# Performance work log

Hardware: AMD Instinct MI355X
Metric: run time of the kernel (lower is better)

The kernel has to match this reference:

```python
import jax, jax.numpy as jnp
import numpy as np

TAU = 1.0
MAX_ITER = 10


def setup_inputs() -> dict:
    key = jax.random.key(0)
    s = jax.random.normal(key, (32, 1024, 1024), dtype=jnp.float32)
    return {"s": s}


def reference(s) -> jnp.ndarray:
    # s: [B, N1, N2] with N1 <= N2 (square here), no padding -> fully vectorized
    log_s = s / TAU
    for i in range(MAX_ITER):
        # even iter: row normalization (logsumexp over columns, axis=2)
        # odd  iter: column normalization (logsumexp over rows, axis=1)
        axis = 2 if i % 2 == 0 else 1
        log_s = log_s - jax.nn.logsumexp(log_s, axis=axis, keepdims=True)
    return jnp.exp(log_s)
```

## Files before the change

kernel.cpp:

```cpp
#include <hip/hip_runtime.h>
#include <math.h>


#define BATCH 32
#define N 1024
#define CHUNKS 8
#define ROWS_PER_CHUNK (N / CHUNKS)

__global__ __launch_bounds__(256) void zero_c_kernel(float* __restrict__ c) {
    int idx = blockIdx.x * 256 + threadIdx.x;
    c[idx] = 0.0f;
}

__global__ __launch_bounds__(256) void row_lse_kernel(const float* __restrict__ s,
                                                      const float* __restrict__ c,
                                                      float* __restrict__ r) {
    const int wave = threadIdx.x >> 6;
    const int lane = threadIdx.x & 63;
    const int row  = blockIdx.x * 4 + wave;
    const int b    = row >> 10;

    const float4* __restrict__ srow = (const float4*)(s + (size_t)row * N);
    const float4* __restrict__ crow = (const float4*)(c + (size_t)b * N);

    float x[16];
#pragma unroll
    for (int k = 0; k < 4; k++) {
        float4 v  = srow[lane + k * 64];
        float4 cv = crow[lane + k * 64];
        x[4 * k + 0] = v.x + cv.x;
        x[4 * k + 1] = v.y + cv.y;
        x[4 * k + 2] = v.z + cv.z;
        x[4 * k + 3] = v.w + cv.w;
    }

    float m = x[0];
#pragma unroll
    for (int t = 1; t < 16; t++) m = fmaxf(m, x[t]);
#pragma unroll
    for (int off = 32; off > 0; off >>= 1) m = fmaxf(m, __shfl_xor(m, off, 64));

    float sum = 0.0f;
#pragma unroll
    for (int t = 0; t < 16; t++) sum += __expf(x[t] - m);
#pragma unroll
    for (int off = 32; off > 0; off >>= 1) sum += __shfl_xor(sum, off, 64);

    if (lane == 0) r[row] = -(m + __logf(sum));
}

__global__ __launch_bounds__(1024) void col_lse_partial_kernel(const float* __restrict__ s,
                                                               const float* __restrict__ r,
                                                               float* __restrict__ pm,
                                                               float* __restrict__ pl) {
    const int bc    = blockIdx.x;
    const int b     = bc >> 3;
    const int chunk = bc & (CHUNKS - 1);
    const int j     = threadIdx.x;

    __shared__ float rs[ROWS_PER_CHUNK];
    if (threadIdx.x < ROWS_PER_CHUNK)
        rs[threadIdx.x] = r[b * N + chunk * ROWS_PER_CHUNK + threadIdx.x];
    __syncthreads();

    const float* __restrict__ base =
        s + ((size_t)(b * N + chunk * ROWS_PER_CHUNK)) * N + j;

    float m = -3.0e38f, l = 0.0f;
#pragma unroll 4
    for (int i = 0; i < ROWS_PER_CHUNK; i++) {
        float x  = base[(size_t)i * N] + rs[i];
        float mn = fmaxf(m, x);
        l = l * __expf(m - mn) + __expf(x - mn);
        m = mn;
    }
    pm[bc * N + j] = m;
    pl[bc * N + j] = l;
}

__global__ __launch_bounds__(1024) void col_combine_kernel(const float* __restrict__ pm,
                                                           const float* __restrict__ pl,
                                                           float* __restrict__ c) {
    const int b = blockIdx.x;
    const int j = threadIdx.x;
    float M = -3.0e38f, L = 0.0f;
#pragma unroll
    for (int chunk = 0; chunk < CHUNKS; chunk++) {
        float m  = pm[(b * CHUNKS + chunk) * N + j];
        float l  = pl[(b * CHUNKS + chunk) * N + j];
        float mn = fmaxf(M, m);
        L = L * __expf(M - mn) + l * __expf(m - mn);
        M = mn;
    }
    c[b * N + j] = -(M + __logf(L));
}

__global__ __launch_bounds__(1024) void col_lse_direct_kernel(const float* __restrict__ s,
                                                              const float* __restrict__ r,
                                                              float* __restrict__ c) {
    const int b = blockIdx.x;
    const int j = threadIdx.x;
    const float* __restrict__ rb = r + b * N;
    const float* __restrict__ base = s + (size_t)b * N * N + j;
    float m = -3.0e38f, l = 0.0f;
    for (int i = 0; i < N; i++) {
        float x  = base[(size_t)i * N] + rb[i];
        float mn = fmaxf(m, x);
        l = l * __expf(m - mn) + __expf(x - mn);
        m = mn;
    }
    c[b * N + j] = -(m + __logf(l));
}

__global__ __launch_bounds__(256) void finalize_kernel(const float* __restrict__ s,
                                                       const float* __restrict__ r,
                                                       const float* __restrict__ c,
                                                       float* __restrict__ out) {
    const int f4  = blockIdx.x * 256 + threadIdx.x;
    const int j4  = f4 & 255;
    const int row = f4 >> 8;
    const int b   = row >> 10;

    float4 v  = ((const float4*)s)[f4];
    float  rr = r[row];
    float4 cc = ((const float4*)c)[(b << 8) + j4];

    float4 o;
    o.x = __expf(v.x + rr + cc.x);
    o.y = __expf(v.y + rr + cc.y);
    o.z = __expf(v.z + rr + cc.z);
    o.w = __expf(v.w + rr + cc.w);
    ((float4*)out)[f4] = o;
}

extern "C" void kernel_launch(void* const* d_in, const int* in_sizes, int n_in,
                              void* d_out, int out_size, void* d_ws, size_t ws_size,
                              hipStream_t stream) {
    const float* s = (const float*)d_in[0];
    float* out = (float*)d_out;

    float* c  = (float*)d_ws;
    float* r  = c + BATCH * N;
    float* pm = r + BATCH * N;
    float* pl = pm + BATCH * CHUNKS * N;

    const size_t needed = (size_t)(2 * BATCH * N + 2 * BATCH * CHUNKS * N) * sizeof(float);
    const bool use_partials = ws_size >= needed;

    zero_c_kernel<<<(BATCH * N) / 256, 256, 0, stream>>>(c);

    for (int it = 0; it < 10; it++) {
        if ((it & 1) == 0) {
            row_lse_kernel<<<(BATCH * N) / 4, 256, 0, stream>>>(s, c, r);
        } else if (use_partials) {
            col_lse_partial_kernel<<<BATCH * CHUNKS, 1024, 0, stream>>>(s, r, pm, pl);
            col_combine_kernel<<<BATCH, 1024, 0, stream>>>(pm, pl, c);
        } else {
            col_lse_direct_kernel<<<BATCH, 1024, 0, stream>>>(s, r, c);
        }
    }

    const int total_f4 = BATCH * N * N / 4;
    finalize_kernel<<<total_f4 / 256, 256, 0, stream>>>(s, r, c, out);
}
```

Baseline: 436.8 us.

## Fuse row LSE with column partial LSE per row-chunk block

Replaces separate row-normalization and column-partial kernels with one kernel per row chunk. It computes row LSEs for 32 rows, keeps them in shared memory, then rereads those rows (likely from cache) to build column partial max/sum with float4 loads. The combine kernel gains more parallelism via an intra-block tree, and the zero-init launch is removed. The workspace requirement grows to 32 partial chunks, and the fallback path becomes the slow direct column kernel.

```diff
diff --git a/kernel.cpp b/kernel.cpp
--- a/kernel.cpp
+++ b/kernel.cpp
@@ -4,12 +4,132 @@
 
 #define BATCH 32
 #define N 1024
-#define CHUNKS 8
-#define ROWS_PER_CHUNK (N / CHUNKS)
+#define RCHUNKS 32
+#define ROWS_PER_BLK 32
+#define BGROUPS 2
+#define ROWS_PER_GROUP 16
+#define PCHUNKS RCHUNKS
+
+__global__ __launch_bounds__(512, 4) void fused_pair_kernel(
+    const float* __restrict__ s, const float* __restrict__ c,
+    float* __restrict__ r, float* __restrict__ pm, float* __restrict__ pl,
+    int has_c)
+{
+    const int bc    = blockIdx.x;
+    const int b     = bc >> 5;
+    const int chunk = bc & 31;
+    const int row0  = chunk * ROWS_PER_BLK;
+
+    __shared__ float cs[N];
+    __shared__ float rs[ROWS_PER_BLK];
+    __shared__ float sm[BGROUPS][N];
+    __shared__ float sl[BGROUPS][N];
+
+    if (has_c) {
+        ((float2*)cs)[threadIdx.x] = ((const float2*)(c + b * N))[threadIdx.x];
+    } else {
+        ((float2*)cs)[threadIdx.x] = make_float2(0.f, 0.f);
+    }
+    __syncthreads();
+
+    const int wave = threadIdx.x >> 6;
+    const int lane = threadIdx.x & 63;
+    const float4* cs4 = (const float4*)cs;
+#pragma unroll
+    for (int rp = 0; rp < 4; rp++) {
+        const int row = wave * 4 + rp;
+        const float4* srow = (const float4*)(s + ((size_t)(b * N + row0 + row)) * N);
+        float x[16];
+#pragma unroll
+        for (int k = 0; k < 4; k++) {
+            float4 v  = srow[lane + 64 * k];
+            float4 cv = cs4[lane + 64 * k];
+            x[4*k+0] = v.x + cv.x; x[4*k+1] = v.y + cv.y;
+            x[4*k+2] = v.z + cv.z; x[4*k+3] = v.w + cv.w;
+        }
+        float m = x[0];
+#pragma unroll
+        for (int t = 1; t < 16; t++) m = fmaxf(m, x[t]);
+#pragma unroll
+        for (int off = 32; off > 0; off >>= 1) m = fmaxf(m, __shfl_xor(m, off, 64));
+        float sum = 0.f;
+#pragma unroll
+        for (int t = 0; t < 16; t++) sum += __expf(x[t] - m);
+#pragma unroll
+        for (int off = 32; off > 0; off >>= 1) sum += __shfl_xor(sum, off, 64);
+        if (lane == 0) {
+            float rv = -(m + __logf(sum));
+            rs[row] = rv;
+            r[b * N + row0 + row] = rv;
+        }
+    }
+    __syncthreads();
+
+    const int j4 = threadIdx.x & 255;
+    const int g  = threadIdx.x >> 8;
+    const float4* sb4 = (const float4*)(s + ((size_t)(b * N + row0 + g * ROWS_PER_GROUP)) * N);
+    float m0=-3.0e38f, m1=-3.0e38f, m2=-3.0e38f, m3=-3.0e38f;
+    float l0=0.f, l1=0.f, l2=0.f, l3=0.f;
+#pragma unroll
+    for (int i = 0; i < ROWS_PER_GROUP; i++) {
+        float ri = rs[g * ROWS_PER_GROUP + i];
+        float4 v = sb4[(size_t)i * 256 + j4];
+        float x0 = v.x + ri, x1 = v.y + ri, x2 = v.z + ri, x3 = v.w + ri;
+        float n0 = fmaxf(m0, x0); l0 = l0 * __expf(m0 - n0) + __expf(x0 - n0); m0 = n0;
+        float n1 = fmaxf(m1, x1); l1 = l1 * __expf(m1 - n1) + __expf(x1 - n1); m1 = n1;
+        float n2 = fmaxf(m2, x2); l2 = l2 * __expf(m2 - n2) + __expf(x2 - n2); m2 = n2;
+        float n3 = fmaxf(m3, x3); l3 = l3 * __expf(m3 - n3) + __expf(x3 - n3); m3 = n3;
+    }
+    ((float4*)sm[g])[j4] = make_float4(m0, m1, m2, m3);
+    ((float4*)sl[g])[j4] = make_float4(l0, l1, l2, l3);
+    __syncthreads();
+
+#pragma unroll
+    for (int cc = 0; cc < 2; cc++) {
+        const int col = threadIdx.x + cc * 512;
+        float M = sm[0][col], L = sl[0][col];
+        float m = sm[1][col], l = sl[1][col];
+        float mn = fmaxf(M, m);
+        L = L * __expf(M - mn) + l * __expf(m - mn);
+        pm[(size_t)bc * N + col] = mn;
+        pl[(size_t)bc * N + col] = L;
+    }
+}
+
+__global__ __launch_bounds__(1024) void col_combine_kernel(
+    const float* __restrict__ pm, const float* __restrict__ pl,
+    float* __restrict__ c)
+{
+    const int b  = blockIdx.x >> 2;
+    const int q  = blockIdx.x & 3;
+    const int jc = threadIdx.x & 255;
+    const int kg = threadIdx.x >> 8;
+    const int j  = q * 256 + jc;
+    float M = -3.0e38f, L = 0.f;
+#pragma unroll
+    for (int k = 0; k < 8; k++) {
+        const int kk = kg * 8 + k;
+        float m = pm[((size_t)(b * PCHUNKS + kk)) * N + j];
+        float l = pl[((size_t)(b * PCHUNKS + kk)) * N + j];
+        float mn = fmaxf(M, m);
+        L = L * __expf(M - mn) + l * __expf(m - mn); M = mn;
+    }
+    __shared__ float smm[4][256], sll[4][256];
+    smm[kg][jc] = M; sll[kg][jc] = L;
+    __syncthreads();
+    if (kg == 0) {
+#pragma unroll
+        for (int g2 = 1; g2 < 4; g2++) {
+            float m = smm[g2][jc], l = sll[g2][jc];
+            float mn = fmaxf(M, m);
+            L = L * __expf(M - mn) + l * __expf(m - mn); M = mn;
+        }
+        c[b * N + j] = -(M + __logf(L));
+    }
+}
 
 __global__ __launch_bounds__(256) void zero_c_kernel(float* __restrict__ c) {
-    int idx = blockIdx.x * 256 + threadIdx.x;
-    c[idx] = 0.0f;
+    c[blockIdx.x * 256 + threadIdx.x] = 0.0f;
 }
 
 __global__ __launch_bounds__(256) void row_lse_kernel(const float* __restrict__ s,
@@ -19,80 +139,26 @@
     const int lane = threadIdx.x & 63;
     const int row  = blockIdx.x * 4 + wave;
     const int b    = row >> 10;
-
-    const float4* __restrict__ srow = (const float4*)(s + (size_t)row * N);
-    const float4* __restrict__ crow = (const float4*)(c + (size_t)b * N);
-
+    const float4* srow = (const float4*)(s + (size_t)row * N);
+    const float4* crow = (const float4*)(c + (size_t)b * N);
     float x[16];
 #pragma unroll
     for (int k = 0; k < 4; k++) {
-        float4 v  = srow[lane + k * 64];
+        float4 v = srow[lane + k * 64];
         float4 cv = crow[lane + k * 64];
-        x[4 * k + 0] = v.x + cv.x;
-        x[4 * k + 1] = v.y + cv.y;
-        x[4 * k + 2] = v.z + cv.z;
-        x[4 * k + 3] = v.w + cv.w;
-    }
-
+        x[4*k+0]=v.x+cv.x; x[4*k+1]=v.y+cv.y; x[4*k+2]=v.z+cv.z; x[4*k+3]=v.w+cv.w;
+    }
     float m = x[0];
 #pragma unroll
     for (int t = 1; t < 16; t++) m = fmaxf(m, x[t]);
 #pragma unroll
     for (int off = 32; off > 0; off >>= 1) m = fmaxf(m, __shfl_xor(m, off, 64));
-
-    float sum = 0.0f;
+    float sum = 0.f;
 #pragma unroll
     for (int t = 0; t < 16; t++) sum += __expf(x[t] - m);
 #pragma unroll
     for (int off = 32; off > 0; off >>= 1) sum += __shfl_xor(sum, off, 64);
-
     if (lane == 0) r[row] = -(m + __logf(sum));
-}
-
-__global__ __launch_bounds__(1024) void col_lse_partial_kernel(const float* __restrict__ s,
-                                                               const float* __restrict__ r,
-                                                               float* __restrict__ pm,
-                                                               float* __restrict__ pl) {
-    const int bc    = blockIdx.x;
-    const int b     = bc >> 3;
-    const int chunk = bc & (CHUNKS - 1);
-    const int j     = threadIdx.x;
-
-    __shared__ float rs[ROWS_PER_CHUNK];
-    if (threadIdx.x < ROWS_PER_CHUNK)
-        rs[threadIdx.x] = r[b * N + chunk * ROWS_PER_CHUNK + threadIdx.x];
-    __syncthreads();
-
-    const float* __restrict__ base =
-        s + ((size_t)(b * N + chunk * ROWS_PER_CHUNK)) * N + j;
-
-    float m = -3.0e38f, l = 0.0f;
-#pragma unroll 4
-    for (int i = 0; i < ROWS_PER_CHUNK; i++) {
-        float x  = base[(size_t)i * N] + rs[i];
-        float mn = fmaxf(m, x);
-        l = l * __expf(m - mn) + __expf(x - mn);
-        m = mn;
-    }
-    pm[bc * N + j] = m;
-    pl[bc * N + j] = l;
-}
-
-__global__ __launch_bounds__(1024) void col_combine_kernel(const float* __restrict__ pm,
-                                                           const float* __restrict__ pl,
-                                                           float* __restrict__ c) {
-    const int b = blockIdx.x;
-    const int j = threadIdx.x;
-    float M = -3.0e38f, L = 0.0f;
-#pragma unroll
-    for (int chunk = 0; chunk < CHUNKS; chunk++) {
-        float m  = pm[(b * CHUNKS + chunk) * N + j];
-        float l  = pl[(b * CHUNKS + chunk) * N + j];
-        float mn = fmaxf(M, m);
-        L = L * __expf(M - mn) + l * __expf(m - mn);
-        M = mn;
-    }
-    c[b * N + j] = -(M + __logf(L));
 }
 
 __global__ __launch_bounds__(1024) void col_lse_direct_kernel(const float* __restrict__ s,
@@ -100,9 +166,9 @@
                                                               float* __restrict__ c) {
     const int b = blockIdx.x;
     const int j = threadIdx.x;
-    const float* __restrict__ rb = r + b * N;
-    const float* __restrict__ base = s + (size_t)b * N * N + j;
-    float m = -3.0e38f, l = 0.0f;
+    const float* rb = r + b * N;
+    const float* base = s + (size_t)b * N * N + j;
+    float m = -3.0e38f, l = 0.f;
     for (int i = 0; i < N; i++) {
         float x  = base[(size_t)i * N] + rb[i];
         float mn = fmaxf(m, x);
@@ -120,11 +186,9 @@
     const int j4  = f4 & 255;
     const int row = f4 >> 8;
     const int b   = row >> 10;
-
     float4 v  = ((const float4*)s)[f4];
     float  rr = r[row];
     float4 cc = ((const float4*)c)[(b << 8) + j4];
-
     float4 o;
     o.x = __expf(v.x + rr + cc.x);
     o.y = __expf(v.y + rr + cc.y);
@@ -142,21 +206,24 @@
     float* c  = (float*)d_ws;
     float* r  = c + BATCH * N;
     float* pm = r + BATCH * N;
-    float* pl = pm + BATCH * CHUNKS * N;
-
-    const size_t needed = (size_t)(2 * BATCH * N + 2 * BATCH * CHUNKS * N) * sizeof(float);
-    const bool use_partials = ws_size >= needed;
-
-    zero_c_kernel<<<(BATCH * N) / 256, 256, 0, stream>>>(c);
-
-    for (int it = 0; it < 10; it++) {
-        if ((it & 1) == 0) {
-            row_lse_kernel<<<(BATCH * N) / 4, 256, 0, stream>>>(s, c, r);
-        } else if (use_partials) {
-            col_lse_partial_kernel<<<BATCH * CHUNKS, 1024, 0, stream>>>(s, r, pm, pl);
-            col_combine_kernel<<<BATCH, 1024, 0, stream>>>(pm, pl, c);
-        } else {
-            col_lse_direct_kernel<<<BATCH, 1024, 0, stream>>>(s, r, c);
+    float* pl = pm + BATCH * PCHUNKS * N;
+
+    const size_t needed =
+        (size_t)(2 * BATCH * N + 2 * BATCH * PCHUNKS * N) * sizeof(float);
+
+    if (ws_size >= needed) {
+        for (int p = 0; p < 5; p++) {
+            fused_pair_kernel<<<BATCH * RCHUNKS, 512, 0, stream>>>(
+                s, c, r, pm, pl, p > 0 ? 1 : 0);
+            col_combine_kernel<<<BATCH * 4, 1024, 0, stream>>>(pm, pl, c);
+        }
+    } else {
+        zero_c_kernel<<<(BATCH * N) / 256, 256, 0, stream>>>(c);
+        for (int it = 0; it < 10; it++) {
+            if ((it & 1) == 0)
+                row_lse_kernel<<<(BATCH * N) / 4, 256, 0, stream>>>(s, c, r);
+            else
+                col_lse_direct_kernel<<<BATCH, 1024, 0, stream>>>(s, r, c);
         }
     }
 
```

Measured after the change: 431.7 us. Within noise of the previous version (-1.2%).

## Replace multi-kernel Sinkhorn loop with a persistent cooperative kernel using grid syncs

Applied to the files above, without the earlier changes.

Fuses all row and column log-sum-exp passes plus the final exp into one cooperative persistent kernel of 1024 blocks. Grid-wide syncs take the place of the roughly 17 separate kernel launches. Each block owns a 32-row by 32-column tile per batch, so the per-chunk data may stay resident in L2/MALL across iterations. Column reductions are combined within the block through shared memory instead of partial buffers and a combine kernel. This depends on all 1024 blocks being co-resident; if the cooperative launch fails, it falls back to the slower direct column kernel path.

```diff
diff --git a/kernel.cpp b/kernel.cpp
--- a/kernel.cpp
+++ b/kernel.cpp
@@ -1,15 +1,129 @@
 #include <hip/hip_runtime.h>
+#include <hip/hip_cooperative_groups.h>
 #include <math.h>
+
+namespace cg = cooperative_groups;
 
 
 #define BATCH 32
 #define N 1024
-#define CHUNKS 8
-#define ROWS_PER_CHUNK (N / CHUNKS)
+#define NBLOCKS 1024
+#define NTHREADS 256
+
+__global__ __launch_bounds__(256, 4) void sinkhorn_persistent(
+    const float* __restrict__ s, float* __restrict__ r, float* __restrict__ c,
+    float* __restrict__ out)
+{
+    cg::grid_group grid = cg::this_grid();
+    const int t     = threadIdx.x;
+    const int b     = blockIdx.x >> 5;
+    const int chunk = blockIdx.x & 31;
+
+    __shared__ float cs[N];
+    __shared__ float rs[N];
+    __shared__ float4 sm[32][8];
+    __shared__ float4 sl[32][8];
+
+    const int wave = t >> 6;
+    const int lane = t & 63;
+
+    for (int it = 0; it < 10; it += 2) {
+        if (it == 0)
+            ((float4*)cs)[t] = make_float4(0.f, 0.f, 0.f, 0.f);
+        else
+            ((float4*)cs)[t] = ((const float4*)(c + b * N))[t];
+        __syncthreads();
+        const float4* cs4 = (const float4*)cs;
+        for (int rp = 0; rp < 8; rp++) {
+            const int row = wave * 8 + rp;
+            const float4* srow =
+                (const float4*)(s + ((size_t)(b * N + chunk * 32 + row)) * N);
+            float x[16];
+#pragma unroll
+            for (int k = 0; k < 4; k++) {
+                float4 v  = srow[lane + 64 * k];
+                float4 cv = cs4[lane + 64 * k];
+                x[4*k+0] = v.x + cv.x; x[4*k+1] = v.y + cv.y;
+                x[4*k+2] = v.z + cv.z; x[4*k+3] = v.w + cv.w;
+            }
+            float m = x[0];
+#pragma unroll
+            for (int q = 1; q < 16; q++) m = fmaxf(m, x[q]);
+#pragma unroll
+            for (int off = 32; off; off >>= 1) m = fmaxf(m, __shfl_xor(m, off, 64));
+            float sum = 0.f;
+#pragma unroll
+            for (int q = 0; q < 16; q++) sum += __expf(x[q] - m);
+#pragma unroll
+            for (int off = 32; off; off >>= 1) sum += __shfl_xor(sum, off, 64);
+            if (lane == 0)
+                r[b * N + chunk * 32 + row] = -(m + __logf(sum));
+        }
+        grid.sync();
+
+        ((float4*)rs)[t] = ((const float4*)(r + b * N))[t];
+        __syncthreads();
+        const int col4 = t & 7;
+        const int rch  = t >> 3;
+        const float4* base =
+            (const float4*)(s + ((size_t)(b * N + rch * 32)) * N) + chunk * 8 + col4;
+        float4 m4 = make_float4(-3e38f, -3e38f, -3e38f, -3e38f);
+        float4 l4 = make_float4(0.f, 0.f, 0.f, 0.f);
+#pragma unroll 4
+        for (int i = 0; i < 32; i++) {
+            float ri = rs[rch * 32 + i];
+            float4 v = base[(size_t)i * 256];
+            float x0 = v.x + ri, x1 = v.y + ri, x2 = v.z + ri, x3 = v.w + ri;
+            float n;
+            n = fmaxf(m4.x, x0); l4.x = l4.x * __expf(m4.x - n) + __expf(x0 - n); m4.x = n;
+            n = fmaxf(m4.y, x1); l4.y = l4.y * __expf(m4.y - n) + __expf(x1 - n); m4.y = n;
+            n = fmaxf(m4.z, x2); l4.z = l4.z * __expf(m4.z - n) + __expf(x2 - n); m4.z = n;
+            n = fmaxf(m4.w, x3); l4.w = l4.w * __expf(m4.w - n) + __expf(x3 - n); m4.w = n;
+        }
+        sm[rch][col4] = m4;
+        sl[rch][col4] = l4;
+        __syncthreads();
+        if (t < 8) {
+            float4 M = sm[0][t], L = sl[0][t];
+#pragma unroll
+            for (int k2 = 1; k2 < 32; k2++) {
+                float4 m2 = sm[k2][t], l2 = sl[k2][t];
+                float n;
+                n = fmaxf(M.x, m2.x); L.x = L.x * __expf(M.x - n) + l2.x * __expf(m2.x - n); M.x = n;
+                n = fmaxf(M.y, m2.y); L.y = L.y * __expf(M.y - n) + l2.y * __expf(m2.y - n); M.y = n;
+                n = fmaxf(M.z, m2.z); L.z = L.z * __expf(M.z - n) + l2.z * __expf(m2.z - n); M.z = n;
+                n = fmaxf(M.w, m2.w); L.w = L.w * __expf(M.w - n) + l2.w * __expf(m2.w - n); M.w = n;
+            }
+            float4 o;
+            o.x = -(M.x + __logf(L.x));
+            o.y = -(M.y + __logf(L.y));
+            o.z = -(M.z + __logf(L.z));
+            o.w = -(M.w + __logf(L.w));
+            ((float4*)(c + b * N + chunk * 32))[t] = o;
+        }
+        grid.sync();
+    }
+
+    ((float4*)cs)[t] = ((const float4*)(c + b * N))[t];
+    if (t < 32) rs[t] = r[b * N + chunk * 32 + t];
+    __syncthreads();
+    const float4* tile  = (const float4*)(s   + ((size_t)(b * N + chunk * 32)) * N);
+    float4*       otile = (float4*)      (out + ((size_t)(b * N + chunk * 32)) * N);
+    const float4 cc = ((const float4*)cs)[t];
+    for (int j = 0; j < 32; j++) {
+        float rr = rs[j];
+        float4 v = tile[j * 256 + t];
+        float4 o;
+        o.x = __expf(v.x + rr + cc.x);
+        o.y = __expf(v.y + rr + cc.y);
+        o.z = __expf(v.z + rr + cc.z);
+        o.w = __expf(v.w + rr + cc.w);
+        otile[j * 256 + t] = o;
+    }
+}
 
 __global__ __launch_bounds__(256) void zero_c_kernel(float* __restrict__ c) {
-    int idx = blockIdx.x * 256 + threadIdx.x;
-    c[idx] = 0.0f;
+    c[blockIdx.x * 256 + threadIdx.x] = 0.0f;
 }
 
 __global__ __launch_bounds__(256) void row_lse_kernel(const float* __restrict__ s,
@@ -19,80 +133,26 @@
     const int lane = threadIdx.x & 63;
     const int row  = blockIdx.x * 4 + wave;
     const int b    = row >> 10;
-
-    const float4* __restrict__ srow = (const float4*)(s + (size_t)row * N);
-    const float4* __restrict__ crow = (const float4*)(c + (size_t)b * N);
-
+    const float4* srow = (const float4*)(s + (size_t)row * N);
+    const float4* crow = (const float4*)(c + (size_t)b * N);
     float x[16];
 #pragma unroll
     for (int k = 0; k < 4; k++) {
-        float4 v  = srow[lane + k * 64];
+        float4 v = srow[lane + k * 64];
         float4 cv = crow[lane + k * 64];
-        x[4 * k + 0] = v.x + cv.x;
-        x[4 * k + 1] = v.y + cv.y;
-        x[4 * k + 2] = v.z + cv.z;
-        x[4 * k + 3] = v.w + cv.w;
-    }
-
+        x[4*k+0]=v.x+cv.x; x[4*k+1]=v.y+cv.y; x[4*k+2]=v.z+cv.z; x[4*k+3]=v.w+cv.w;
+    }
     float m = x[0];
 #pragma unroll
-    for (int t = 1; t < 16; t++) m = fmaxf(m, x[t]);
-#pragma unroll
-    for (int off = 32; off > 0; off >>= 1) m = fmaxf(m, __shfl_xor(m, off, 64));
-
-    float sum = 0.0f;
-#pragma unroll
-    for (int t = 0; t < 16; t++) sum += __expf(x[t] - m);
-#pragma unroll
-    for (int off = 32; off > 0; off >>= 1) sum += __shfl_xor(sum, off, 64);
-
+    for (int q = 1; q < 16; q++) m = fmaxf(m, x[q]);
+#pragma unroll
+    for (int off = 32; off; off >>= 1) m = fmaxf(m, __shfl_xor(m, off, 64));
+    float sum = 0.f;
+#pragma unroll
+    for (int q = 0; q < 16; q++) sum += __expf(x[q] - m);
+#pragma unroll
+    for (int off = 32; off; off >>= 1) sum += __shfl_xor(sum, off, 64);
     if (lane == 0) r[row] = -(m + __logf(sum));
-}
-
-__global__ __launch_bounds__(1024) void col_lse_partial_kernel(const float* __restrict__ s,
-                                                               const float* __restrict__ r,
-                                                               float* __restrict__ pm,
-                                                               float* __restrict__ pl) {
-    const int bc    = blockIdx.x;
-    const int b     = bc >> 3;
-    const int chunk = bc & (CHUNKS - 1);
-    const int j     = threadIdx.x;
-
-    __shared__ float rs[ROWS_PER_CHUNK];
-    if (threadIdx.x < ROWS_PER_CHUNK)
-        rs[threadIdx.x] = r[b * N + chunk * ROWS_PER_CHUNK + threadIdx.x];
-    __syncthreads();
-
-    const float* __restrict__ base =
-        s + ((size_t)(b * N + chunk * ROWS_PER_CHUNK)) * N + j;
-
-    float m = -3.0e38f, l = 0.0f;
-#pragma unroll 4
-    for (int i = 0; i < ROWS_PER_CHUNK; i++) {
-        float x  = base[(size_t)i * N] + rs[i];
-        float mn = fmaxf(m, x);
-        l = l * __expf(m - mn) + __expf(x - mn);
-        m = mn;
-    }
-    pm[bc * N + j] = m;
-    pl[bc * N + j] = l;
-}
-
-__global__ __launch_bounds__(1024) void col_combine_kernel(const float* __restrict__ pm,
-                                                           const float* __restrict__ pl,
-                                                           float* __restrict__ c) {
-    const int b = blockIdx.x;
-    const int j = threadIdx.x;
-    float M = -3.0e38f, L = 0.0f;
-#pragma unroll
-    for (int chunk = 0; chunk < CHUNKS; chunk++) {
-        float m  = pm[(b * CHUNKS + chunk) * N + j];
-        float l  = pl[(b * CHUNKS + chunk) * N + j];
-        float mn = fmaxf(M, m);
-        L = L * __expf(M - mn) + l * __expf(m - mn);
-        M = mn;
-    }
-    c[b * N + j] = -(M + __logf(L));
 }
 
 __global__ __launch_bounds__(1024) void col_lse_direct_kernel(const float* __restrict__ s,
@@ -100,9 +160,9 @@
                                                               float* __restrict__ c) {
     const int b = blockIdx.x;
     const int j = threadIdx.x;
-    const float* __restrict__ rb = r + b * N;
-    const float* __restrict__ base = s + (size_t)b * N * N + j;
-    float m = -3.0e38f, l = 0.0f;
+    const float* rb = r + b * N;
+    const float* base = s + (size_t)b * N * N + j;
+    float m = -3.0e38f, l = 0.f;
     for (int i = 0; i < N; i++) {
         float x  = base[(size_t)i * N] + rb[i];
         float mn = fmaxf(m, x);
@@ -120,11 +180,9 @@
     const int j4  = f4 & 255;
     const int row = f4 >> 8;
     const int b   = row >> 10;
-
     float4 v  = ((const float4*)s)[f4];
     float  rr = r[row];
     float4 cc = ((const float4*)c)[(b << 8) + j4];
-
     float4 o;
     o.x = __expf(v.x + rr + cc.x);
     o.y = __expf(v.y + rr + cc.y);
@@ -138,28 +196,22 @@
                               hipStream_t stream) {
     const float* s = (const float*)d_in[0];
     float* out = (float*)d_out;
-
-    float* c  = (float*)d_ws;
-    float* r  = c + BATCH * N;
-    float* pm = r + BATCH * N;
-    float* pl = pm + BATCH * CHUNKS * N;
-
-    const size_t needed = (size_t)(2 * BATCH * N + 2 * BATCH * CHUNKS * N) * sizeof(float);
-    const bool use_partials = ws_size >= needed;
-
-    zero_c_kernel<<<(BATCH * N) / 256, 256, 0, stream>>>(c);
-
-    for (int it = 0; it < 10; it++) {
-        if ((it & 1) == 0) {
-            row_lse_kernel<<<(BATCH * N) / 4, 256, 0, stream>>>(s, c, r);
-        } else if (use_partials) {
-            col_lse_partial_kernel<<<BATCH * CHUNKS, 1024, 0, stream>>>(s, r, pm, pl);
-            col_combine_kernel<<<BATCH, 1024, 0, stream>>>(pm, pl, c);
-        } else {
-            col_lse_direct_kernel<<<BATCH, 1024, 0, stream>>>(s, r, c);
-        }
-    }
-
-    const int total_f4 = BATCH * N * N / 4;
-    finalize_kernel<<<total_f4 / 256, 256, 0, stream>>>(s, r, c, out);
-}
+    float* c = (float*)d_ws;
+    float* r = c + BATCH * N;
+
+    void* args[] = { (void*)&s, (void*)&r, (void*)&c, (void*)&out };
+    hipError_t err = hipLaunchCooperativeKernel(
+        (void*)sinkhorn_persistent, dim3(NBLOCKS), dim3(NTHREADS), args, 0, stream);
+
+    if (err != hipSuccess) {
+        zero_c_kernel<<<(BATCH * N) / 256, 256, 0, stream>>>(c);
+        for (int it = 0; it < 10; it++) {
+            if ((it & 1) == 0)
+                row_lse_kernel<<<(BATCH * N) / 4, 256, 0, stream>>>(s, c, r);
+            else
+                col_lse_direct_kernel<<<BATCH, 1024, 0, stream>>>(s, r, c);
+        }
+        const int total_f4 = BATCH * N * N / 4;
+        finalize_kernel<<<total_f4 / 256, 256, 0, stream>>>(s, r, c, out);
+    }
+}
```

New measurement: 1.498 ms. 3.43x slower.
